# Kernel optimization log

Hardware: AMD Instinct MI355X
Metric: run time of the kernel (lower is better)

## Reference

```python
import jax, jax.numpy as jnp
import numpy as np

EMBED_DIM = 512
NUM_HEADS = 32


def setup_inputs() -> dict:
    key = jax.random.key(0)
    ks = jax.random.split(key, 12)
    n_node, bsz, E = 512, 4, EMBED_DIM
    s = 0.02
    return {
        "query": jax.random.normal(ks[0], (n_node, bsz, E), jnp.float32),
        "attn_bias": jax.random.normal(ks[1], (bsz, NUM_HEADS, n_node, n_node), jnp.float32),
        "delta_pos": jax.random.normal(ks[2], (bsz, n_node, n_node, 3), jnp.float32),
        "Wq": jax.random.normal(ks[3], (E, E), jnp.float32) * s,
        "bq": jnp.zeros((E,), jnp.float32),
        "Wk": jax.random.normal(ks[4], (E, E), jnp.float32) * s,
        "bk": jnp.zeros((E,), jnp.float32),
        "Wv": jax.random.normal(ks[5], (E, E), jnp.float32) * s,
        "bv": jnp.zeros((E,), jnp.float32),
        "Wf": jax.random.normal(ks[6], (3, E), jnp.float32) * s,  # force_proj1..3 weights
        "bf": jnp.zeros((3,), jnp.float32),
    }


def reference(query, attn_bias, delta_pos, Wq, bq, Wk, bk, Wv, bv, Wf, bf):
    # query: [n_node, bsz, E] -> [bsz, n_node, E]
    x = jnp.transpose(query, (1, 0, 2))
    bsz, n, E = x.shape
    h = NUM_HEADS
    d = E // h
    scaling = d ** (-0.5)
    # projections (torch Linear: x @ W.T + b), split heads -> [b, h, n, d]
    q = (x @ Wq.T + bq).reshape(bsz, n, h, d).transpose(0, 2, 1, 3) * scaling
    k = (x @ Wk.T + bk).reshape(bsz, n, h, d).transpose(0, 2, 1, 3)
    v = (x @ Wv.T + bv).reshape(bsz, n, h, d).transpose(0, 2, 1, 3)
    attn = jnp.einsum('bhid,bhjd->bhij', q, k)  # [b,h,n,n]
    probs = jax.nn.softmax(attn + attn_bias, axis=-1)  # dropout in eval mode = identity
    # x[b,i,c,h,d] = sum_j probs[b,h,i,j] * delta_pos[b,i,j,c] * v[b,h,j,d]
    xo = jnp.einsum('bhij,bijc,bhjd->bichd', probs, delta_pos, v)
    xo = xo.reshape(bsz, n, 3, E)  # matches permute(0,3,2,1,4).view(b,n,3,h*d)
    # per-axis force projections to scalar
    force = jnp.einsum('bnce,ce->bnc', xo, Wf) + bf  # [b,n,3]
    return force.astype(jnp.float32)
```

## Files before the change

kernel.cpp:

```cpp
#include <hip/hip_runtime.h>
#include <hip/hip_bf16.h>


__global__ __launch_bounds__(256) void wvf_prep(
    const float* __restrict__ Wv, const float* __restrict__ Wf,
    const float* __restrict__ bv, float* __restrict__ Wvf,
    float* __restrict__ bvf)
{
    int idx = blockIdx.x * 256 + threadIdx.x;
    int k = idx & 511, o = idx >> 9;
    float acc = 0.f;
    if (o < 96) {
        int h = o / 3, c = o % 3;
        #pragma unroll
        for (int d = 0; d < 16; ++d)
            acc += Wf[c * 512 + h * 16 + d] * Wv[(h * 16 + d) * 512 + k];
    }
    Wvf[o * 512 + k] = acc;
    if (k == 0) {
        float bacc = 0.f;
        if (o < 96) {
            int h = o / 3, c = o % 3;
            #pragma unroll
            for (int d = 0; d < 16; ++d)
                bacc += Wf[c * 512 + h * 16 + d] * bv[h * 16 + d];
        }
        bvf[o] = bacc;
    }
}

__global__ __launch_bounds__(256) void proj_all(
    const float* __restrict__ query,
    const float* __restrict__ Wq, const float* __restrict__ bq,
    const float* __restrict__ Wk, const float* __restrict__ bk,
    const float* __restrict__ Wvf, const float* __restrict__ bvf,
    float* __restrict__ Qp, float* __restrict__ Kp, float* __restrict__ wvT)
{
    __shared__ float As[64 * 16];
    __shared__ float Bst[16][68];
    const int tid = threadIdx.x;
    const int tx = tid & 15, ty = tid >> 4;
    const int xs = blockIdx.x;
    const int sel = (xs >= 16) ? 2 : (xs >= 8 ? 1 : 0);
    const float* __restrict__ W    = sel == 0 ? Wq : sel == 1 ? Wk : Wvf;
    const float* __restrict__ bias = sel == 0 ? bq : sel == 1 ? bk : bvf;
    const float scale = sel == 0 ? 0.25f : 1.0f;
    const int c0 = (sel == 0 ? xs : sel == 1 ? xs - 8 : xs - 16) * 64;
    const int row0 = blockIdx.y * 64;
    const int b = blockIdx.z;

    const int lr = tid >> 2, lk4 = tid & 3;
    float acc[4][4] = {};

    for (int kt = 0; kt < 512; kt += 16) {
        {
            int r = lr, k4 = lk4;
            float4 av = *(const float4*)&query[((size_t)(row0 + r) * 4 + b) * 512 + kt + k4 * 4];
            int slot = k4 ^ ((r >> 2) & 3);
            *(float4*)&As[r * 16 + slot * 4] = av;
            float4 bv4 = *(const float4*)&W[(size_t)(c0 + r) * 512 + kt + k4 * 4];
            Bst[k4 * 4 + 0][r] = bv4.x;
            Bst[k4 * 4 + 1][r] = bv4.y;
            Bst[k4 * 4 + 2][r] = bv4.z;
            Bst[k4 * 4 + 3][r] = bv4.w;
        }
        __syncthreads();
        #pragma unroll
        for (int k4 = 0; k4 < 4; ++k4) {
            float4 a4[4];
            const int slot = k4 ^ (ty & 3);
            #pragma unroll
            for (int i = 0; i < 4; ++i)
                a4[i] = *(const float4*)&As[(ty * 4 + i) * 16 + slot * 4];
            #pragma unroll
            for (int kk = 0; kk < 4; ++kk) {
                float4 b4 = *(const float4*)&Bst[k4 * 4 + kk][tx * 4];
                #pragma unroll
                for (int i = 0; i < 4; ++i) {
                    float a = (kk == 0) ? a4[i].x : (kk == 1) ? a4[i].y
                             : (kk == 2) ? a4[i].z : a4[i].w;
                    acc[i][0] += a * b4.x;
                    acc[i][1] += a * b4.y;
                    acc[i][2] += a * b4.z;
                    acc[i][3] += a * b4.w;
                }
            }
        }
        __syncthreads();
    }

    if (sel < 2) {
        float* __restrict__ C = sel == 0 ? Qp : Kp;
        #pragma unroll
        for (int i = 0; i < 4; ++i) {
            int row = row0 + ty * 4 + i, col = c0 + tx * 4;
            float4 o;
            o.x = (acc[i][0] + bias[col + 0]) * scale;
            o.y = (acc[i][1] + bias[col + 1]) * scale;
            o.z = (acc[i][2] + bias[col + 2]) * scale;
            o.w = (acc[i][3] + bias[col + 3]) * scale;
            *(float4*)&C[(size_t)b * 262144 + (size_t)row * 512 + col] = o;
        }
    } else {
        #pragma unroll
        for (int i = 0; i < 4; ++i) {
            int row = row0 + ty * 4 + i;
            #pragma unroll
            for (int j = 0; j < 4; ++j) {
                int col = c0 + tx * 4 + j;
                wvT[(size_t)b * 65536 + (size_t)col * 512 + row] = acc[i][j] + bias[col];
            }
        }
    }
}

__global__ __launch_bounds__(256, 4) void attn_force(
    const float* __restrict__ Q, const float* __restrict__ K,
    const float* __restrict__ wvT, const float* __restrict__ abias,
    const float* __restrict__ delta, const float* __restrict__ bf,
    float* __restrict__ force)
{
    __shared__ float4 kbuf4[4 * 512];
    __shared__ float qs[16][16];

    const int tid = threadIdx.x;
    const int l = tid & 63, w = tid >> 6;
    const int bid = blockIdx.x;
    const int wid = (bid & 7) * 512 + (bid >> 3);
    const int b = wid >> 10;
    const int it = (wid >> 5) & 31;
    const int h = wid & 31;
    const int i0 = it * 16;
    const int m = l & 7;

    #pragma unroll
    for (int s = 0; s < 8; ++s) {
        int idx = s * 256 + tid;
        int j = idx >> 2, d4 = idx & 3;
        float4 kv = *(const float4*)&K[(size_t)(b * 512 + j) * 512 + h * 16 + d4 * 4];
        kbuf4[d4 * 512 + (j ^ ((j >> 3) & 7))] = kv;
    }
    if (tid < 64) {
        int r = tid >> 2, d4 = tid & 3;
        *(float4*)&qs[r][d4 * 4] =
            *(const float4*)&Q[(size_t)(b * 512 + i0 + r) * 512 + h * 16 + d4 * 4];
    }

    const size_t bbase = (size_t)(b * 32 + h) * 262144;
    const int row_w = i0 + w * 4;
    float4 A0[4], A1[4];
    #pragma unroll
    for (int rr = 0; rr < 4; ++rr) {
        const float* ab = &abias[bbase + (size_t)(row_w + rr) * 512 + l * 8];
        A0[rr] = *(const float4*)&ab[0];
        A1[rr] = *(const float4*)&ab[4];
    }
    __syncthreads();

    float sc[4][8];
    #pragma unroll
    for (int rr = 0; rr < 4; ++rr) {
        sc[rr][0] = A0[rr].x; sc[rr][1] = A0[rr].y;
        sc[rr][2] = A0[rr].z; sc[rr][3] = A0[rr].w;
        sc[rr][4] = A1[rr].x; sc[rr][5] = A1[rr].y;
        sc[rr][6] = A1[rr].z; sc[rr][7] = A1[rr].w;
    }

    #pragma unroll
    for (int d4 = 0; d4 < 4; ++d4) {
        float4 q4[4];
        #pragma unroll
        for (int rr = 0; rr < 4; ++rr)
            q4[rr] = *(const float4*)&qs[w * 4 + rr][d4 * 4];
        #pragma unroll
        for (int jj = 0; jj < 8; ++jj) {
            float4 kv = kbuf4[d4 * 512 + 8 * l + (jj ^ m)];
            #pragma unroll
            for (int rr = 0; rr < 4; ++rr)
                sc[rr][jj] += q4[rr].x * kv.x + q4[rr].y * kv.y +
                              q4[rr].z * kv.z + q4[rr].w * kv.w;
        }
    }

    const float* wvb = &wvT[(size_t)(b * 128 + h * 3) * 512];
    float wvf[3][8];
    #pragma unroll
    for (int c = 0; c < 3; ++c) {
        float4 a = *(const float4*)&wvb[c * 512 + l * 8];
        float4 bq4 = *(const float4*)&wvb[c * 512 + l * 8 + 4];
        wvf[c][0] = a.x;  wvf[c][1] = a.y;  wvf[c][2] = a.z;  wvf[c][3] = a.w;
        wvf[c][4] = bq4.x; wvf[c][5] = bq4.y; wvf[c][6] = bq4.z; wvf[c][7] = bq4.w;
    }

    #pragma unroll
    for (int rr = 0; rr < 4; ++rr) {
        float mx = sc[rr][0];
        #pragma unroll
        for (int jj = 1; jj < 8; ++jj) mx = fmaxf(mx, sc[rr][jj]);
        #pragma unroll
        for (int off = 32; off >= 1; off >>= 1)
            mx = fmaxf(mx, __shfl_xor(mx, off));
        float sum = 0.f;
        #pragma unroll
        for (int jj = 0; jj < 8; ++jj) {
            float p = __expf(sc[rr][jj] - mx);
            sc[rr][jj] = p;
            sum += p;
        }
        #pragma unroll
        for (int off = 32; off >= 1; off >>= 1)
            sum += __shfl_xor(sum, off);
        float inv = 1.0f / sum;
        #pragma unroll
        for (int jj = 0; jj < 8; ++jj) sc[rr][jj] *= inv;
    }

    float f[4][3] = {};
    #pragma unroll
    for (int rr = 0; rr < 4; ++rr) {
        const float* dbase = &delta[((size_t)(b * 512 + row_w + rr) * 512 + l * 8) * 3];
        float dd[24];
        #pragma unroll
        for (int q6 = 0; q6 < 6; ++q6) {
            float4 dv = *(const float4*)&dbase[q6 * 4];
            dd[q6 * 4 + 0] = dv.x; dd[q6 * 4 + 1] = dv.y;
            dd[q6 * 4 + 2] = dv.z; dd[q6 * 4 + 3] = dv.w;
        }
        #pragma unroll
        for (int jj = 0; jj < 8; ++jj) {
            float p = sc[rr][jj];
            f[rr][0] += p * wvf[0][jj] * dd[3 * jj + 0];
            f[rr][1] += p * wvf[1][jj] * dd[3 * jj + 1];
            f[rr][2] += p * wvf[2][jj] * dd[3 * jj + 2];
        }
    }

    #pragma unroll
    for (int rr = 0; rr < 4; ++rr)
        #pragma unroll
        for (int c = 0; c < 3; ++c) {
            float v = f[rr][c];
            #pragma unroll
            for (int off = 32; off >= 1; off >>= 1)
                v += __shfl_xor(v, off);
            f[rr][c] = v;
        }
    if (l == 0) {
        #pragma unroll
        for (int rr = 0; rr < 4; ++rr) {
            int row = row_w + rr;
            #pragma unroll
            for (int c = 0; c < 3; ++c) {
                float v = f[rr][c];
                if (h == 0) v += bf[c];
                atomicAdd(&force[(size_t)(b * 512 + row) * 3 + c], v);
            }
        }
    }
}

extern "C" void kernel_launch(void* const* d_in, const int* in_sizes, int n_in,
                              void* d_out, int out_size, void* d_ws, size_t ws_size,
                              hipStream_t stream)
{
    const float* query = (const float*)d_in[0];
    const float* abias = (const float*)d_in[1];
    const float* delta = (const float*)d_in[2];
    const float* Wq    = (const float*)d_in[3];
    const float* bq    = (const float*)d_in[4];
    const float* Wk    = (const float*)d_in[5];
    const float* bk    = (const float*)d_in[6];
    const float* Wv    = (const float*)d_in[7];
    const float* bv    = (const float*)d_in[8];
    const float* Wf    = (const float*)d_in[9];
    const float* bf    = (const float*)d_in[10];

    float* ws  = (float*)d_ws;
    float* Qp  = ws;
    float* Kp  = ws + 1048576;
    float* wvT = ws + 2097152;
    float* Wvf = ws + 2359296;
    float* bvf = ws + 2424832;

    hipMemsetAsync(d_out, 0, (size_t)out_size * sizeof(float), stream);

    wvf_prep<<<256, 256, 0, stream>>>(Wv, Wf, bv, Wvf, bvf);

    proj_all<<<dim3(18, 8, 4), 256, 0, stream>>>(query, Wq, bq, Wk, bk,
                                                 Wvf, bvf, Qp, Kp, wvT);

    attn_force<<<4096, 256, 0, stream>>>(Qp, Kp, wvT, abias, delta, bf,
                                         (float*)d_out);
}
```

Before: 337.9 us.

## Store K as bf16 in LDS, double-buffer projection GEMM, raise occupancy hint

The attention kernel now rounds K to bf16 and stores it packed in shared memory, halving LDS use per block so the launch bound can allow 5 blocks per CU. Scores are still accumulated in fp32. Separately, the projection GEMM gets register-staged double buffering of its shared-memory tiles, so global loads for the next k-tile overlap compute on the current one. The bf16 K rounding adds numerical error to the attention logits, and the extra buffers and raised occupancy bound may add register pressure or spills.

```diff
diff --git a/kernel.cpp b/kernel.cpp
--- a/kernel.cpp
+++ b/kernel.cpp
@@ -1,6 +1,11 @@
 #include <hip/hip_runtime.h>
 #include <hip/hip_bf16.h>
 
+
+__device__ __forceinline__ unsigned int rne_bf16(float x) {
+    unsigned int b = __float_as_uint(x);
+    return (b + 0x7fffu + ((b >> 16) & 1u)) >> 16;
+}
 
 __global__ __launch_bounds__(256) void wvf_prep(
     const float* __restrict__ Wv, const float* __restrict__ Wf,
@@ -36,8 +41,8 @@
     const float* __restrict__ Wvf, const float* __restrict__ bvf,
     float* __restrict__ Qp, float* __restrict__ Kp, float* __restrict__ wvT)
 {
-    __shared__ float As[64 * 16];
-    __shared__ float Bst[16][68];
+    __shared__ float As[2][64 * 16];
+    __shared__ float Bst[2][16][68];
     const int tid = threadIdx.x;
     const int tx = tid & 15, ty = tid >> 4;
     const int xs = blockIdx.x;
@@ -50,31 +55,41 @@
     const int b = blockIdx.z;
 
     const int lr = tid >> 2, lk4 = tid & 3;
+    const int slot = lk4 ^ ((lr >> 2) & 3);
+    const size_t abase = ((size_t)(row0 + lr) * 4 + b) * 512 + lk4 * 4;
+    const size_t bbase = (size_t)(c0 + lr) * 512 + lk4 * 4;
+
     float acc[4][4] = {};
 
-    for (int kt = 0; kt < 512; kt += 16) {
-        {
-            int r = lr, k4 = lk4;
-            float4 av = *(const float4*)&query[((size_t)(row0 + r) * 4 + b) * 512 + kt + k4 * 4];
-            int slot = k4 ^ ((r >> 2) & 3);
-            *(float4*)&As[r * 16 + slot * 4] = av;
-            float4 bv4 = *(const float4*)&W[(size_t)(c0 + r) * 512 + kt + k4 * 4];
-            Bst[k4 * 4 + 0][r] = bv4.x;
-            Bst[k4 * 4 + 1][r] = bv4.y;
-            Bst[k4 * 4 + 2][r] = bv4.z;
-            Bst[k4 * 4 + 3][r] = bv4.w;
-        }
-        __syncthreads();
+    {
+        float4 av = *(const float4*)&query[abase];
+        float4 bw = *(const float4*)&W[bbase];
+        *(float4*)&As[0][lr * 16 + slot * 4] = av;
+        Bst[0][lk4 * 4 + 0][lr] = bw.x;
+        Bst[0][lk4 * 4 + 1][lr] = bw.y;
+        Bst[0][lk4 * 4 + 2][lr] = bw.z;
+        Bst[0][lk4 * 4 + 3][lr] = bw.w;
+    }
+    __syncthreads();
+
+    for (int it = 0; it < 32; ++it) {
+        const int cur = it & 1;
+        float4 av_n, bw_n;
+        if (it < 31) {
+            int kt = (it + 1) * 16;
+            av_n = *(const float4*)&query[abase + kt];
+            bw_n = *(const float4*)&W[bbase + kt];
+        }
         #pragma unroll
         for (int k4 = 0; k4 < 4; ++k4) {
             float4 a4[4];
-            const int slot = k4 ^ (ty & 3);
+            const int rslot = k4 ^ (ty & 3);
             #pragma unroll
             for (int i = 0; i < 4; ++i)
-                a4[i] = *(const float4*)&As[(ty * 4 + i) * 16 + slot * 4];
+                a4[i] = *(const float4*)&As[cur][(ty * 4 + i) * 16 + rslot * 4];
             #pragma unroll
             for (int kk = 0; kk < 4; ++kk) {
-                float4 b4 = *(const float4*)&Bst[k4 * 4 + kk][tx * 4];
+                float4 b4 = *(const float4*)&Bst[cur][k4 * 4 + kk][tx * 4];
                 #pragma unroll
                 for (int i = 0; i < 4; ++i) {
                     float a = (kk == 0) ? a4[i].x : (kk == 1) ? a4[i].y
@@ -87,6 +102,14 @@
             }
         }
         __syncthreads();
+        if (it < 31) {
+            *(float4*)&As[cur ^ 1][lr * 16 + slot * 4] = av_n;
+            Bst[cur ^ 1][lk4 * 4 + 0][lr] = bw_n.x;
+            Bst[cur ^ 1][lk4 * 4 + 1][lr] = bw_n.y;
+            Bst[cur ^ 1][lk4 * 4 + 2][lr] = bw_n.z;
+            Bst[cur ^ 1][lk4 * 4 + 3][lr] = bw_n.w;
+        }
+        __syncthreads();
     }
 
     if (sel < 2) {
@@ -114,13 +137,13 @@
     }
 }
 
-__global__ __launch_bounds__(256, 4) void attn_force(
+__global__ __launch_bounds__(256, 5) void attn_force(
     const float* __restrict__ Q, const float* __restrict__ K,
     const float* __restrict__ wvT, const float* __restrict__ abias,
     const float* __restrict__ delta, const float* __restrict__ bf,
     float* __restrict__ force)
 {
-    __shared__ float4 kbuf4[4 * 512];
+    __shared__ unsigned int kb[4096];
     __shared__ float qs[16][16];
 
     const int tid = threadIdx.x;
@@ -131,14 +154,16 @@
     const int it = (wid >> 5) & 31;
     const int h = wid & 31;
     const int i0 = it * 16;
-    const int m = l & 7;
 
     #pragma unroll
     for (int s = 0; s < 8; ++s) {
         int idx = s * 256 + tid;
         int j = idx >> 2, d4 = idx & 3;
         float4 kv = *(const float4*)&K[(size_t)(b * 512 + j) * 512 + h * 16 + d4 * 4];
-        kbuf4[d4 * 512 + (j ^ ((j >> 3) & 7))] = kv;
+        unsigned int u0 = rne_bf16(kv.x) | (rne_bf16(kv.y) << 16);
+        unsigned int u1 = rne_bf16(kv.z) | (rne_bf16(kv.w) << 16);
+        int byte = (j * 32 + d4 * 8) ^ (((j >> 3) & 7) << 4);
+        *(uint2*)((char*)kb + byte) = make_uint2(u0, u1);
     }
     if (tid < 64) {
         int r = tid >> 2, d4 = tid & 3;
@@ -166,19 +191,30 @@
         sc[rr][6] = A1[rr].z; sc[rr][7] = A1[rr].w;
     }
 
-    #pragma unroll
-    for (int d4 = 0; d4 < 4; ++d4) {
-        float4 q4[4];
-        #pragma unroll
-        for (int rr = 0; rr < 4; ++rr)
-            q4[rr] = *(const float4*)&qs[w * 4 + rr][d4 * 4];
+    const int sw = (l & 7) << 4;
+    #pragma unroll
+    for (int hf = 0; hf < 2; ++hf) {
+        float qh[4][8];
+        #pragma unroll
+        for (int rr = 0; rr < 4; ++rr) {
+            float4 qa = *(const float4*)&qs[w * 4 + rr][hf * 8];
+            float4 qb = *(const float4*)&qs[w * 4 + rr][hf * 8 + 4];
+            qh[rr][0] = qa.x; qh[rr][1] = qa.y; qh[rr][2] = qa.z; qh[rr][3] = qa.w;
+            qh[rr][4] = qb.x; qh[rr][5] = qb.y; qh[rr][6] = qb.z; qh[rr][7] = qb.w;
+        }
         #pragma unroll
         for (int jj = 0; jj < 8; ++jj) {
-            float4 kv = kbuf4[d4 * 512 + 8 * l + (jj ^ m)];
+            int byte = ((8 * l + jj) * 32 + hf * 16) ^ sw;
+            uint4 u = *(const uint4*)((const char*)kb + byte);
+            float k0 = __uint_as_float(u.x << 16), k1 = __uint_as_float(u.x & 0xffff0000u);
+            float k2 = __uint_as_float(u.y << 16), k3 = __uint_as_float(u.y & 0xffff0000u);
+            float k4 = __uint_as_float(u.z << 16), k5 = __uint_as_float(u.z & 0xffff0000u);
+            float k6 = __uint_as_float(u.w << 16), k7 = __uint_as_float(u.w & 0xffff0000u);
             #pragma unroll
             for (int rr = 0; rr < 4; ++rr)
-                sc[rr][jj] += q4[rr].x * kv.x + q4[rr].y * kv.y +
-                              q4[rr].z * kv.z + q4[rr].w * kv.w;
+                sc[rr][jj] += qh[rr][0] * k0 + qh[rr][1] * k1 + qh[rr][2] * k2 +
+                              qh[rr][3] * k3 + qh[rr][4] * k4 + qh[rr][5] * k5 +
+                              qh[rr][6] * k6 + qh[rr][7] * k7;
         }
     }
 
```

Result: faster. 328.5 us (-2.8%).
